# Optimization experiments

Hardware: AMD Instinct MI355X
Metric: run time of the kernel (lower is better)

Reference implementation:

```python
import jax, jax.numpy as jnp
import numpy as np

D_MODEL = 768
N_HEADS = 12
HEAD_DIM = D_MODEL // N_HEADS
D_FF = 4 * D_MODEL
EPS = 1e-5


def setup_inputs() -> dict:
    key = jax.random.key(0)
    ks = jax.random.split(key, 16)
    s = 0.02
    x = jax.random.normal(ks[0], (2, 2048, D_MODEL), dtype=jnp.float32)
    wq = jax.random.normal(ks[1], (D_MODEL, D_MODEL), dtype=jnp.float32) * s
    bq = jnp.zeros((D_MODEL,), jnp.float32)
    wk = jax.random.normal(ks[2], (D_MODEL, D_MODEL), dtype=jnp.float32) * s
    bk = jnp.zeros((D_MODEL,), jnp.float32)
    wv = jax.random.normal(ks[3], (D_MODEL, D_MODEL), dtype=jnp.float32) * s
    bv = jnp.zeros((D_MODEL,), jnp.float32)
    wo = jax.random.normal(ks[4], (D_MODEL, D_MODEL), dtype=jnp.float32) * s
    bo = jnp.zeros((D_MODEL,), jnp.float32)
    w1 = jax.random.normal(ks[5], (D_MODEL, D_FF), dtype=jnp.float32) * s
    b1 = jnp.zeros((D_FF,), jnp.float32)
    w2 = jax.random.normal(ks[6], (D_FF, D_MODEL), dtype=jnp.float32) * s
    b2 = jnp.zeros((D_MODEL,), jnp.float32)
    ln1_g = jnp.ones((D_MODEL,), jnp.float32)
    ln1_b = jnp.zeros((D_MODEL,), jnp.float32)
    ln2_g = jnp.ones((D_MODEL,), jnp.float32)
    ln2_b = jnp.zeros((D_MODEL,), jnp.float32)
    return dict(x=x, wq=wq, bq=bq, wk=wk, bk=bk, wv=wv, bv=bv, wo=wo, bo=bo,
                w1=w1, b1=b1, w2=w2, b2=b2,
                ln1_g=ln1_g, ln1_b=ln1_b, ln2_g=ln2_g, ln2_b=ln2_b)


def _layernorm(x, g, b):
    mu = jnp.mean(x, axis=-1, keepdims=True)
    var = jnp.mean(jnp.square(x - mu), axis=-1, keepdims=True)
    return (x - mu) * jax.lax.rsqrt(var + EPS) * g + b


def _attention(x, wq, bq, wk, bk, wv, bv, wo, bo):
    B, S, D = x.shape
    def split_heads(t):  # [B,S,D] -> [B,H,S,Hd]
        return t.reshape(B, S, N_HEADS, HEAD_DIM).transpose(0, 2, 1, 3)
    q = split_heads(x @ wq + bq)
    k = split_heads(x @ wk + bk)
    v = split_heads(x @ wv + bv)
    scores = jnp.einsum('bhqd,bhkd->bhqk', q, k) / np.sqrt(HEAD_DIM).astype(np.float32)
    causal = jnp.tril(jnp.ones((S, S), dtype=bool))
    scores = jnp.where(causal, scores, -jnp.inf)
    weights = jax.nn.softmax(scores, axis=-1)
    attn = jnp.einsum('bhqk,bhkd->bhqd', weights, v)
    attn = attn.transpose(0, 2, 1, 3).reshape(B, S, D)
    return attn @ wo + bo


def reference(x, wq, bq, wk, bk, wv, bv, wo, bo, w1, b1, w2, b2,
              ln1_g, ln1_b, ln2_g, ln2_b):
    x = x + _attention(_layernorm(x, ln1_g, ln1_b), wq, bq, wk, bk, wv, bv, wo, bo)
    h = _layernorm(x, ln2_g, ln2_b)
    ff = jax.nn.relu(h @ w1 + b1) @ w2 + b2
    return x + ff
```

## Files before the change

### kernel.cpp

```cpp
#include <hip/hip_runtime.h>
#include <stdint.h>

typedef __bf16 bf16;
typedef float f32x4 __attribute__((ext_vector_type(4)));
typedef bf16 bf16x8 __attribute__((ext_vector_type(8)));
typedef bf16 bf16x4 __attribute__((ext_vector_type(4)));

#define MFMA16(a, b, c) __builtin_amdgcn_mfma_f32_16x16x32_bf16((a), (b), (c), 0, 0, 0)

static __device__ __forceinline__ void load_lds16(const bf16* g, bf16* l) {
  __builtin_amdgcn_global_load_lds(
      (const __attribute__((address_space(1))) void*)g,
      (__attribute__((address_space(3))) void*)l, 16, 0, 0);
}

static __device__ __forceinline__ float fast_exp2(float x) {
#if __has_builtin(__builtin_amdgcn_exp2f)
  return __builtin_amdgcn_exp2f(x);
#else
  return exp2f(x);
#endif
}

__global__ void __launch_bounds__(256) k_transpose(
    const float* s0, const float* s1, const float* s2, const float* s3,
    const float* s4, const float* s5,
    bf16* d0, bf16* d1, bf16* d2, bf16* d3, bf16* d4, bf16* d5) {
  int z = blockIdx.z;
  const float* src; bf16* dst; int R, C;
  switch (z) {
    case 0: src = s0; dst = d0; R = 768;  C = 768;  break;
    case 1: src = s1; dst = d1; R = 768;  C = 768;  break;
    case 2: src = s2; dst = d2; R = 768;  C = 768;  break;
    case 3: src = s3; dst = d3; R = 768;  C = 768;  break;
    case 4: src = s4; dst = d4; R = 768;  C = 3072; break;
    default: src = s5; dst = d5; R = 3072; C = 768; break;
  }
  int tcn = C >> 5;
  int nt = (R >> 5) * tcn;
  int t = blockIdx.x;
  if (t >= nt) return;
  int tr = t / tcn, tc = t % tcn;
  __shared__ float tile[32][33];
  int tx = threadIdx.x & 31, ty = threadIdx.x >> 5;
  for (int i = 0; i < 4; i++)
    tile[ty + i * 8][tx] = src[(size_t)(tr * 32 + ty + i * 8) * C + tc * 32 + tx];
  __syncthreads();
  for (int i = 0; i < 4; i++)
    dst[(size_t)(tc * 32 + ty + i * 8) * R + tr * 32 + tx] = (bf16)tile[tx][ty + i * 8];
}

__global__ void __launch_bounds__(256) k_layernorm(
    const float* __restrict__ in, const float* __restrict__ gam,
    const float* __restrict__ bet, bf16* __restrict__ out) {
  int row = blockIdx.x, tid = threadIdx.x;
  const float* rp = in + (size_t)row * 768;
  float v0 = rp[tid], v1 = rp[tid + 256], v2 = rp[tid + 512];
  float s = v0 + v1 + v2, sq = v0 * v0 + v1 * v1 + v2 * v2;
  for (int off = 1; off < 64; off <<= 1) {
    s += __shfl_xor(s, off, 64);
    sq += __shfl_xor(sq, off, 64);
  }
  __shared__ float ps[8];
  if ((tid & 63) == 0) { ps[tid >> 6] = s; ps[4 + (tid >> 6)] = sq; }
  __syncthreads();
  s = ps[0] + ps[1] + ps[2] + ps[3];
  sq = ps[4] + ps[5] + ps[6] + ps[7];
  float mu = s * (1.0f / 768.0f);
  float rstd = rsqrtf(sq * (1.0f / 768.0f) - mu * mu + 1e-5f);
  bf16* op = out + (size_t)row * 768;
  op[tid] = (bf16)((v0 - mu) * rstd * gam[tid] + bet[tid]);
  op[tid + 256] = (bf16)((v1 - mu) * rstd * gam[tid + 256] + bet[tid + 256]);
  op[tid + 512] = (bf16)((v2 - mu) * rstd * gam[tid + 512] + bet[tid + 512]);
}

__global__ void __launch_bounds__(256) k_ln2_reduce(
    const bf16* __restrict__ p0, const bf16* __restrict__ p1,
    const bf16* __restrict__ p2, const bf16* __restrict__ p3,
    const float* __restrict__ x, const float* __restrict__ bo,
    const float* __restrict__ gam, const float* __restrict__ bet,
    float* __restrict__ x1, bf16* __restrict__ h2) {
  int row = blockIdx.x, tid = threadIdx.x;
  size_t base = (size_t)row * 768;
  float v0, v1, v2;
  {
    size_t c = base + tid;
    v0 = (float)p0[c] + (float)p1[c] + (float)p2[c] + (float)p3[c] + x[c] + bo[tid];
    c = base + tid + 256;
    v1 = (float)p0[c] + (float)p1[c] + (float)p2[c] + (float)p3[c] + x[c] + bo[tid + 256];
    c = base + tid + 512;
    v2 = (float)p0[c] + (float)p1[c] + (float)p2[c] + (float)p3[c] + x[c] + bo[tid + 512];
  }
  x1[base + tid] = v0; x1[base + tid + 256] = v1; x1[base + tid + 512] = v2;
  float s = v0 + v1 + v2, sq = v0 * v0 + v1 * v1 + v2 * v2;
  for (int off = 1; off < 64; off <<= 1) {
    s += __shfl_xor(s, off, 64);
    sq += __shfl_xor(sq, off, 64);
  }
  __shared__ float ps[8];
  if ((tid & 63) == 0) { ps[tid >> 6] = s; ps[4 + (tid >> 6)] = sq; }
  __syncthreads();
  s = ps[0] + ps[1] + ps[2] + ps[3];
  sq = ps[4] + ps[5] + ps[6] + ps[7];
  float mu = s * (1.0f / 768.0f);
  float rstd = rsqrtf(sq * (1.0f / 768.0f) - mu * mu + 1e-5f);
  bf16* op = h2 + base;
  op[tid] = (bf16)((v0 - mu) * rstd * gam[tid] + bet[tid]);
  op[tid + 256] = (bf16)((v1 - mu) * rstd * gam[tid + 256] + bet[tid + 256]);
  op[tid + 512] = (bf16)((v2 - mu) * rstd * gam[tid + 512] + bet[tid + 512]);
}

static __device__ __forceinline__ f32x4 cvt4(const bf16* p, size_t i) {
  bf16x4 v = *(const bf16x4*)(p + i);
  f32x4 r;
  for (int j = 0; j < 4; j++) r[j] = (float)v[j];
  return r;
}

__global__ void __launch_bounds__(256) k_ff2_reduce(
    const bf16* __restrict__ f0, const bf16* __restrict__ f1,
    const bf16* __restrict__ f2, const bf16* __restrict__ f3,
    const float* __restrict__ x1, const float* __restrict__ b2,
    float* __restrict__ out) {
  size_t i = ((size_t)blockIdx.x * 256 + threadIdx.x) * 4;
  int col = (int)(i % 768);
  f32x4 v = *(const f32x4*)(x1 + i);
  f32x4 b = *(const f32x4*)(b2 + col);
  f32x4 r = v + b + cvt4(f0, i) + cvt4(f1, i) + cvt4(f2, i) + cvt4(f3, i);
  *(f32x4*)(out + i) = r;
}

static __device__ __forceinline__ void gemm_core(
    const bf16* __restrict__ A, int lda, const bf16* __restrict__ Bt, int ldb,
    int Kc, int m0, int n0, bf16* As, bf16* Bs, f32x4 acc[4][4]) {
  int tid = threadIdx.x, w = tid >> 6, lane = tid & 63, quad = lane >> 4, l15 = lane & 15;
  int wr = w >> 1, wc = w & 1;
  int srow = lane & 15, skc = (lane >> 4) * 8;
  const bf16* ga[2];
  const bf16* gb[2];
  for (int c = 0; c < 2; c++) {
    int seg = w * 2 + c;
    ga[c] = A + (size_t)(m0 + seg * 16 + srow) * lda + skc;
    gb[c] = Bt + (size_t)(n0 + seg * 16 + srow) * ldb + skc;
  }
  bf16x8 rA[2][2], rB[2][2];
  for (int c = 0; c < 2; c++)
    for (int h = 0; h < 2; h++) {
      rA[c][h] = *(const bf16x8*)(ga[c] + h * 32);
      rB[c][h] = *(const bf16x8*)(gb[c] + h * 32);
    }
  int k0 = 0;
  while (true) {
    for (int c = 0; c < 2; c++) {
      int seg = w * 2 + c;
      for (int h = 0; h < 2; h++) {
        *(bf16x8*)(As + seg * 1024 + h * 512 + lane * 8) = rA[c][h];
        *(bf16x8*)(Bs + seg * 1024 + h * 512 + lane * 8) = rB[c][h];
      }
    }
    __syncthreads();
    bool more = (k0 + 64) < Kc;
    if (more) {
      for (int c = 0; c < 2; c++)
        for (int h = 0; h < 2; h++) {
          rA[c][h] = *(const bf16x8*)(ga[c] + k0 + 64 + h * 32);
          rB[c][h] = *(const bf16x8*)(gb[c] + k0 + 64 + h * 32);
        }
    }
    for (int ks = 0; ks < 2; ks++) {
      bf16x8 af[4], bfr[4];
      for (int mi = 0; mi < 4; mi++)
        af[mi] = *(const bf16x8*)(As + (wr * 4 + mi) * 1024 + ks * 512 + quad * 128 + l15 * 8);
      for (int ni = 0; ni < 4; ni++)
        bfr[ni] = *(const bf16x8*)(Bs + (wc * 4 + ni) * 1024 + ks * 512 + quad * 128 + l15 * 8);
      for (int mi = 0; mi < 4; mi++)
        for (int ni = 0; ni < 4; ni++)
          acc[mi][ni] = MFMA16(af[mi], bfr[ni], acc[mi][ni]);
    }
    k0 += 64;
    if (!more) break;
    __syncthreads();
  }
}

__global__ void __launch_bounds__(256) k_gemm_relu(
    const bf16* __restrict__ A, const bf16* __restrict__ Bt,
    const float* __restrict__ bias, bf16* __restrict__ outp, int K_, int N_) {
  __shared__ __align__(16) bf16 As[128 * 64];
  __shared__ __align__(16) bf16 Bs[128 * 64];
  int m0 = blockIdx.y * 128, n0 = blockIdx.x * 128;
  f32x4 acc[4][4] = {};
  gemm_core(A, K_, Bt, K_, K_, m0, n0, As, Bs, acc);
  int tid = threadIdx.x, w = tid >> 6, lane = tid & 63, quad = lane >> 4, l15 = lane & 15;
  int wr = w >> 1, wc = w & 1;
  float bv[4];
  for (int ni = 0; ni < 4; ni++) bv[ni] = bias[n0 + wc * 64 + ni * 16 + l15];
  for (int mi = 0; mi < 4; mi++) {
    int mb = m0 + wr * 64 + mi * 16 + quad * 4;
    for (int ni = 0; ni < 4; ni++) {
      int n = n0 + wc * 64 + ni * 16 + l15;
      for (int r = 0; r < 4; r++)
        outp[(size_t)(mb + r) * N_ + n] = (bf16)fmaxf(acc[mi][ni][r] + bv[ni], 0.0f);
    }
  }
}

__global__ void __launch_bounds__(256) k_gemm_split(
    const bf16* __restrict__ A, const bf16* __restrict__ Bt,
    bf16* __restrict__ f0, bf16* __restrict__ f1,
    bf16* __restrict__ f2, bf16* __restrict__ f3, int K_, int Kc, int N_) {
  __shared__ __align__(16) bf16 As[128 * 64];
  __shared__ __align__(16) bf16 Bs[128 * 64];
  int z = blockIdx.z;
  bf16* outp = (z == 0) ? f0 : (z == 1) ? f1 : (z == 2) ? f2 : f3;
  int m0 = blockIdx.y * 128, n0 = blockIdx.x * 128;
  f32x4 acc[4][4] = {};
  gemm_core(A + (size_t)z * Kc, K_, Bt + (size_t)z * Kc, K_, Kc, m0, n0, As, Bs, acc);
  int tid = threadIdx.x, w = tid >> 6, lane = tid & 63, quad = lane >> 4, l15 = lane & 15;
  int wr = w >> 1, wc = w & 1;
  for (int mi = 0; mi < 4; mi++) {
    int mb = m0 + wr * 64 + mi * 16 + quad * 4;
    for (int ni = 0; ni < 4; ni++) {
      int n = n0 + wc * 64 + ni * 16 + l15;
      for (int r = 0; r < 4; r++)
        outp[(size_t)(mb + r) * N_ + n] = (bf16)acc[mi][ni][r];
    }
  }
}

__global__ void __launch_bounds__(256) k_gemm_qkv(
    const bf16* __restrict__ h1, const bf16* __restrict__ wqT,
    const bf16* __restrict__ wkT, const bf16* __restrict__ wvT,
    const float* __restrict__ bq, const float* __restrict__ bk,
    const float* __restrict__ bv, bf16* __restrict__ qb,
    bf16* __restrict__ kb, bf16* __restrict__ vtb) {
  __shared__ __align__(16) bf16 As[128 * 64];
  __shared__ __align__(16) bf16 Bs[128 * 64];
  int z = blockIdx.z;
  const bf16* Bt = (z == 0) ? wqT : (z == 1) ? wkT : wvT;
  const float* bias = (z == 0) ? bq : (z == 1) ? bk : bv;
  int m0 = blockIdx.y * 128, n0 = blockIdx.x * 128;
  f32x4 acc[4][4] = {};
  gemm_core(h1, 768, Bt, 768, 768, m0, n0, As, Bs, acc);
  int tid = threadIdx.x, w = tid >> 6, lane = tid & 63, quad = lane >> 4, l15 = lane & 15;
  int wr = w >> 1, wc = w & 1;
  float bvv[4];
  for (int ni = 0; ni < 4; ni++) bvv[ni] = bias[n0 + wc * 64 + ni * 16 + l15];
  for (int mi = 0; mi < 4; mi++) {
    int mb = m0 + wr * 64 + mi * 16 + quad * 4;
    int b = mb >> 11, s0_ = mb & 2047;
    for (int ni = 0; ni < 4; ni++) {
      int n = n0 + wc * 64 + ni * 16 + l15;
      int h = n >> 6, hd = n & 63;
      if (z < 2) {
        bf16* outp = (z == 0) ? qb : kb;
        size_t base = (size_t)(b * 12 + h) * 2048 * 64;
        for (int r = 0; r < 4; r++)
          outp[base + (size_t)(s0_ + r) * 64 + hd] = (bf16)(acc[mi][ni][r] + bvv[ni]);
      } else {
        bf16x4 pk;
        for (int r = 0; r < 4; r++) pk[r] = (bf16)(acc[mi][ni][r] + bvv[ni]);
        *(bf16x4*)(vtb + (((size_t)(b * 12 + h) * 64 + hd) * 2048 + s0_)) = pk;
      }
    }
  }
}

__global__ void __launch_bounds__(256) k_attn(
    const bf16* __restrict__ qb, const bf16* __restrict__ kb,
    const bf16* __restrict__ vtb, bf16* __restrict__ out) {
  __shared__ __align__(16) bf16 Ks[128 * 64];
  __shared__ __align__(16) bf16 Vs[64 * 128];
  __shared__ __align__(16) bf16 Ps[4][16 * 128];
  int qt = 31 - (blockIdx.x / 24);
  int bh = blockIdx.x % 24;
  int q0 = qt * 64;
  int tid = threadIdx.x, w = tid >> 6, lane = tid & 63, quad = lane >> 4, l15 = lane & 15;
  const bf16* qbase = qb + (size_t)bh * 2048 * 64;
  const bf16* kbase = kb + (size_t)bh * 2048 * 64;
  const bf16* vbase = vtb + (size_t)bh * 64 * 2048;

  bf16x8 qf[2];
  for (int ds = 0; ds < 2; ds++)
    qf[ds] = *(const bf16x8*)(qbase + (size_t)(q0 + w * 16 + l15) * 64 + ds * 32 + quad * 8);

  f32x4 o[4] = {};
  f32x4 l_i = {};

  const float C2 = 0.18033688011112042f;
  int nkt = (qt >> 1) + 1;
  for (int kt = 0; kt < nkt; kt++) {
    int k0 = kt * 128;
    __syncthreads();
    {
      int rsub = lane >> 3, c8 = lane & 7;
      for (int c = 0; c < 4; c++) {
        int seg = c * 4 + w;
        int row = seg * 8 + rsub;
        load_lds16(kbase + (size_t)(k0 + row) * 64 + ((c8 ^ (row & 7)) * 8), Ks + seg * 512);
      }
      int rsub2 = lane >> 4, c16 = lane & 15;
      for (int c = 0; c < 4; c++) {
        int seg = c * 4 + w;
        int row = seg * 4 + rsub2;
        load_lds16(vbase + (size_t)row * 2048 + k0 + ((c16 ^ (row & 15)) * 8), Vs + seg * 512);
      }
    }
    __syncthreads();

    f32x4 sc[8] = {};
    for (int kj = 0; kj < 8; kj++) {
      int krow = kj * 16 + l15;
      for (int ds = 0; ds < 2; ds++) {
        bf16x8 kf = *(const bf16x8*)(Ks + krow * 64 + (((ds * 4 + quad) ^ (krow & 7)) * 8));
        sc[kj] = MFMA16(qf[ds], kf, sc[kj]);
      }
    }
    if (kt == nkt - 1) {
      int qg = q0 + w * 16 + quad * 4;
      for (int kj = 0; kj < 8; kj++) {
        int kg = k0 + kj * 16 + l15;
        for (int r = 0; r < 4; r++)
          if (kg > qg + r) sc[kj][r] = -3.0e38f;
      }
    }
    for (int kj = 0; kj < 8; kj++)
      for (int r = 0; r < 4; r++) {
        float p = fast_exp2(sc[kj][r] * C2);
        sc[kj][r] = p;
        l_i[r] += p;
      }
    for (int kj = 0; kj < 8; kj++) {
      int colb = kj * 16 + l15;
      int chb = colb >> 3, cin = colb & 7;
      for (int r = 0; r < 4; r++) {
        int prow = quad * 4 + r;
        Ps[w][prow * 128 + ((chb ^ prow) * 8) + cin] = (bf16)sc[kj][r];
      }
    }
    for (int ks = 0; ks < 4; ks++) {
      int prow = l15;
      bf16x8 pf = *(const bf16x8*)(&Ps[w][prow * 128 + (((ks * 4 + quad) ^ prow) * 8)]);
      for (int dj = 0; dj < 4; dj++) {
        int vrow = dj * 16 + l15;
        bf16x8 vf = *(const bf16x8*)(Vs + vrow * 128 + (((ks * 4 + quad) ^ (vrow & 15)) * 8));
        o[dj] = MFMA16(pf, vf, o[dj]);
      }
    }
  }
  for (int off = 1; off < 16; off <<= 1)
    for (int r = 0; r < 4; r++) l_i[r] += __shfl_xor(l_i[r], off, 64);
  int b = bh / 12, h = bh % 12;
  f32x4 rl;
  for (int r = 0; r < 4; r++) rl[r] = 1.0f / l_i[r];
  int srow = q0 + w * 16 + quad * 4;
  for (int dj = 0; dj < 4; dj++) {
    int d = h * 64 + dj * 16 + l15;
    for (int r = 0; r < 4; r++)
      out[(size_t)(b * 2048 + srow + r) * 768 + d] = (bf16)(o[dj][r] * rl[r]);
  }
}

extern "C" void kernel_launch(void* const* d_in, const int* in_sizes, int n_in,
                              void* d_out, int out_size, void* d_ws, size_t ws_size,
                              hipStream_t stream) {
  const float* x    = (const float*)d_in[0];
  const float* wq   = (const float*)d_in[1];
  const float* bq   = (const float*)d_in[2];
  const float* wk   = (const float*)d_in[3];
  const float* bk   = (const float*)d_in[4];
  const float* wv   = (const float*)d_in[5];
  const float* bv   = (const float*)d_in[6];
  const float* wo   = (const float*)d_in[7];
  const float* bo   = (const float*)d_in[8];
  const float* w1   = (const float*)d_in[9];
  const float* b1   = (const float*)d_in[10];
  const float* w2   = (const float*)d_in[11];
  const float* b2   = (const float*)d_in[12];
  const float* ln1g = (const float*)d_in[13];
  const float* ln1b = (const float*)d_in[14];
  const float* ln2g = (const float*)d_in[15];
  const float* ln2b = (const float*)d_in[16];

  char* p = (char*)d_ws;
  bf16* wqT = (bf16*)p; p += (size_t)768 * 768 * 2;
  bf16* wkT = (bf16*)p; p += (size_t)768 * 768 * 2;
  bf16* wvT = (bf16*)p; p += (size_t)768 * 768 * 2;
  bf16* woT = (bf16*)p; p += (size_t)768 * 768 * 2;
  bf16* w1T = (bf16*)p; p += (size_t)768 * 3072 * 2;
  bf16* w2T = (bf16*)p; p += (size_t)768 * 3072 * 2;
  bf16* h1   = (bf16*)p; p += (size_t)4096 * 768 * 2;
  bf16* qbuf = (bf16*)p; p += (size_t)4096 * 768 * 2;
  bf16* kbuf = (bf16*)p; p += (size_t)4096 * 768 * 2;
  bf16* vtb  = (bf16*)p; p += (size_t)4096 * 768 * 2;
  bf16* att  = (bf16*)p; p += (size_t)4096 * 768 * 2;
  float* x1  = (float*)p; p += (size_t)4096 * 768 * 4;
  bf16* h2   = (bf16*)p; p += (size_t)4096 * 768 * 2;
  bf16* ffm  = (bf16*)p; p += (size_t)4096 * 3072 * 2;
  bf16* pex  = (bf16*)p; p += (size_t)4096 * 768 * 2;
  bf16* p0 = h1;
  bf16* p1 = qbuf;
  bf16* p2 = kbuf;
  bf16* p3 = pex;
  bf16* f0 = h1; bf16* f1 = qbuf; bf16* f2 = kbuf; bf16* f3 = vtb;

  k_transpose<<<dim3(2304, 1, 6), dim3(256), 0, stream>>>(
      wq, wk, wv, wo, w1, w2, wqT, wkT, wvT, woT, w1T, w2T);
  k_layernorm<<<dim3(4096), dim3(256), 0, stream>>>(x, ln1g, ln1b, h1);
  k_gemm_qkv<<<dim3(6, 32, 3), dim3(256), 0, stream>>>(
      h1, wqT, wkT, wvT, bq, bk, bv, qbuf, kbuf, vtb);
  k_attn<<<dim3(768), dim3(256), 0, stream>>>(qbuf, kbuf, vtb, att);
  k_gemm_split<<<dim3(6, 32, 4), dim3(256), 0, stream>>>(
      att, woT, p0, p1, p2, p3, 768, 192, 768);
  k_ln2_reduce<<<dim3(4096), dim3(256), 0, stream>>>(
      p0, p1, p2, p3, x, bo, ln2g, ln2b, x1, h2);
  k_gemm_relu<<<dim3(24, 32), dim3(256), 0, stream>>>(
      h2, w1T, b1, ffm, 768, 3072);
  k_gemm_split<<<dim3(6, 32, 4), dim3(256), 0, stream>>>(
      ffm, w2T, f0, f1, f2, f3, 3072, 768, 768);
  k_ff2_reduce<<<dim3(3072), dim3(256), 0, stream>>>(
      f0, f1, f2, f3, x1, b2, (float*)d_out);
}
```

Before: 317.0 us.

## Fuse LN1 into prep, fuse FF2 split-K reduce via atomic counters, remap blocks per XCD

Folds the first layernorm into the weight-transpose launch as an extra grid slice, removing one launch. The FF2 split-K reduction moves into the GEMM itself: the last of the four K-split blocks per tile, detected with an atomic counter, sums the partials with the residual and bias. Launch overhead and the separate reduce pass go away, at the cost of fences and atomics; the counters are reset inside the relu GEMM. All GEMMs switch to a 1D grid with an XCD-aware tile mapping so blocks that share A rows land on the same XCD for L2 reuse.

```diff
diff --git a/kernel.cpp b/kernel.cpp
--- a/kernel.cpp
+++ b/kernel.cpp
@@ -22,11 +22,35 @@
 #endif
 }
 
-__global__ void __launch_bounds__(256) k_transpose(
+__global__ void __launch_bounds__(256) k_prep(
     const float* s0, const float* s1, const float* s2, const float* s3,
     const float* s4, const float* s5,
-    bf16* d0, bf16* d1, bf16* d2, bf16* d3, bf16* d4, bf16* d5) {
+    bf16* d0, bf16* d1, bf16* d2, bf16* d3, bf16* d4, bf16* d5,
+    const float* x, const float* ln1g, const float* ln1b, bf16* h1) {
   int z = blockIdx.z;
+  int tid = threadIdx.x;
+  if (z == 6) {
+    int row = blockIdx.x;
+    const float* rp = x + (size_t)row * 768;
+    float v0 = rp[tid], v1 = rp[tid + 256], v2 = rp[tid + 512];
+    float s = v0 + v1 + v2, sq = v0 * v0 + v1 * v1 + v2 * v2;
+    for (int off = 1; off < 64; off <<= 1) {
+      s += __shfl_xor(s, off, 64);
+      sq += __shfl_xor(sq, off, 64);
+    }
+    __shared__ float ps[8];
+    if ((tid & 63) == 0) { ps[tid >> 6] = s; ps[4 + (tid >> 6)] = sq; }
+    __syncthreads();
+    s = ps[0] + ps[1] + ps[2] + ps[3];
+    sq = ps[4] + ps[5] + ps[6] + ps[7];
+    float mu = s * (1.0f / 768.0f);
+    float rstd = rsqrtf(sq * (1.0f / 768.0f) - mu * mu + 1e-5f);
+    bf16* op = h1 + (size_t)row * 768;
+    op[tid] = (bf16)((v0 - mu) * rstd * ln1g[tid] + ln1b[tid]);
+    op[tid + 256] = (bf16)((v1 - mu) * rstd * ln1g[tid + 256] + ln1b[tid + 256]);
+    op[tid + 512] = (bf16)((v2 - mu) * rstd * ln1g[tid + 512] + ln1b[tid + 512]);
+    return;
+  }
   const float* src; bf16* dst; int R, C;
   switch (z) {
     case 0: src = s0; dst = d0; R = 768;  C = 768;  break;
@@ -42,36 +66,12 @@
   if (t >= nt) return;
   int tr = t / tcn, tc = t % tcn;
   __shared__ float tile[32][33];
-  int tx = threadIdx.x & 31, ty = threadIdx.x >> 5;
+  int tx = tid & 31, ty = tid >> 5;
   for (int i = 0; i < 4; i++)
     tile[ty + i * 8][tx] = src[(size_t)(tr * 32 + ty + i * 8) * C + tc * 32 + tx];
   __syncthreads();
   for (int i = 0; i < 4; i++)
     dst[(size_t)(tc * 32 + ty + i * 8) * R + tr * 32 + tx] = (bf16)tile[tx][ty + i * 8];
-}
-
-__global__ void __launch_bounds__(256) k_layernorm(
-    const float* __restrict__ in, const float* __restrict__ gam,
-    const float* __restrict__ bet, bf16* __restrict__ out) {
-  int row = blockIdx.x, tid = threadIdx.x;
-  const float* rp = in + (size_t)row * 768;
-  float v0 = rp[tid], v1 = rp[tid + 256], v2 = rp[tid + 512];
-  float s = v0 + v1 + v2, sq = v0 * v0 + v1 * v1 + v2 * v2;
-  for (int off = 1; off < 64; off <<= 1) {
-    s += __shfl_xor(s, off, 64);
-    sq += __shfl_xor(sq, off, 64);
-  }
-  __shared__ float ps[8];
-  if ((tid & 63) == 0) { ps[tid >> 6] = s; ps[4 + (tid >> 6)] = sq; }
-  __syncthreads();
-  s = ps[0] + ps[1] + ps[2] + ps[3];
-  sq = ps[4] + ps[5] + ps[6] + ps[7];
-  float mu = s * (1.0f / 768.0f);
-  float rstd = rsqrtf(sq * (1.0f / 768.0f) - mu * mu + 1e-5f);
-  bf16* op = out + (size_t)row * 768;
-  op[tid] = (bf16)((v0 - mu) * rstd * gam[tid] + bet[tid]);
-  op[tid + 256] = (bf16)((v1 - mu) * rstd * gam[tid + 256] + bet[tid + 256]);
-  op[tid + 512] = (bf16)((v2 - mu) * rstd * gam[tid + 512] + bet[tid + 512]);
 }
 
 __global__ void __launch_bounds__(256) k_ln2_reduce(
@@ -110,26 +110,6 @@
   op[tid + 512] = (bf16)((v2 - mu) * rstd * gam[tid + 512] + bet[tid + 512]);
 }
 
-static __device__ __forceinline__ f32x4 cvt4(const bf16* p, size_t i) {
-  bf16x4 v = *(const bf16x4*)(p + i);
-  f32x4 r;
-  for (int j = 0; j < 4; j++) r[j] = (float)v[j];
-  return r;
-}
-
-__global__ void __launch_bounds__(256) k_ff2_reduce(
-    const bf16* __restrict__ f0, const bf16* __restrict__ f1,
-    const bf16* __restrict__ f2, const bf16* __restrict__ f3,
-    const float* __restrict__ x1, const float* __restrict__ b2,
-    float* __restrict__ out) {
-  size_t i = ((size_t)blockIdx.x * 256 + threadIdx.x) * 4;
-  int col = (int)(i % 768);
-  f32x4 v = *(const f32x4*)(x1 + i);
-  f32x4 b = *(const f32x4*)(b2 + col);
-  f32x4 r = v + b + cvt4(f0, i) + cvt4(f1, i) + cvt4(f2, i) + cvt4(f3, i);
-  *(f32x4*)(out + i) = r;
-}
-
 static __device__ __forceinline__ void gemm_core(
     const bf16* __restrict__ A, int lda, const bf16* __restrict__ Bt, int ldb,
     int Kc, int m0, int n0, bf16* As, bf16* Bs, f32x4 acc[4][4]) {
@@ -185,10 +165,14 @@
 
 __global__ void __launch_bounds__(256) k_gemm_relu(
     const bf16* __restrict__ A, const bf16* __restrict__ Bt,
-    const float* __restrict__ bias, bf16* __restrict__ outp, int K_, int N_) {
+    const float* __restrict__ bias, bf16* __restrict__ outp,
+    int* __restrict__ cnt, int K_, int N_) {
+  if (blockIdx.x < 192) cnt[blockIdx.x] = 0;
   __shared__ __align__(16) bf16 As[128 * 64];
   __shared__ __align__(16) bf16 Bs[128 * 64];
-  int m0 = blockIdx.y * 128, n0 = blockIdx.x * 128;
+  int l = blockIdx.x, xcd = l & 7, i = l >> 3;
+  int m0 = ((xcd << 2) | (i & 3)) * 128;
+  int n0 = (i >> 2) * 128;
   f32x4 acc[4][4] = {};
   gemm_core(A, K_, Bt, K_, K_, m0, n0, As, Bs, acc);
   int tid = threadIdx.x, w = tid >> 6, lane = tid & 63, quad = lane >> 4, l15 = lane & 15;
@@ -211,9 +195,12 @@
     bf16* __restrict__ f2, bf16* __restrict__ f3, int K_, int Kc, int N_) {
   __shared__ __align__(16) bf16 As[128 * 64];
   __shared__ __align__(16) bf16 Bs[128 * 64];
-  int z = blockIdx.z;
+  int l = blockIdx.x, xcd = l & 7, i = l >> 3;
+  int m0 = ((xcd << 2) | (i & 3)) * 128;
+  int rest = i >> 2;
+  int n0 = (rest % 6) * 128;
+  int z = rest / 6;
   bf16* outp = (z == 0) ? f0 : (z == 1) ? f1 : (z == 2) ? f2 : f3;
-  int m0 = blockIdx.y * 128, n0 = blockIdx.x * 128;
   f32x4 acc[4][4] = {};
   gemm_core(A + (size_t)z * Kc, K_, Bt + (size_t)z * Kc, K_, Kc, m0, n0, As, Bs, acc);
   int tid = threadIdx.x, w = tid >> 6, lane = tid & 63, quad = lane >> 4, l15 = lane & 15;
@@ -225,6 +212,66 @@
       for (int r = 0; r < 4; r++)
         outp[(size_t)(mb + r) * N_ + n] = (bf16)acc[mi][ni][r];
     }
+  }
+}
+
+__global__ void __launch_bounds__(256) k_gemm_ff2(
+    const bf16* __restrict__ A, const bf16* __restrict__ Bt,
+    bf16* __restrict__ f0, bf16* __restrict__ f1,
+    bf16* __restrict__ f2, bf16* __restrict__ f3,
+    const float* __restrict__ x1, const float* __restrict__ b2,
+    float* __restrict__ out, int* __restrict__ cnt, int K_, int Kc, int N_) {
+  __shared__ __align__(16) bf16 As[128 * 64];
+  __shared__ __align__(16) bf16 Bs[128 * 64];
+  int l = blockIdx.x, xcd = l & 7, i = l >> 3;
+  int m_t = (xcd << 2) | (i & 3);
+  int rest = i >> 2;
+  int n_t = rest % 6;
+  int z = rest / 6;
+  int m0 = m_t * 128, n0 = n_t * 128;
+  bf16* outp = (z == 0) ? f0 : (z == 1) ? f1 : (z == 2) ? f2 : f3;
+  f32x4 acc[4][4] = {};
+  gemm_core(A + (size_t)z * Kc, K_, Bt + (size_t)z * Kc, K_, Kc, m0, n0, As, Bs, acc);
+  int tid = threadIdx.x, w = tid >> 6, lane = tid & 63, quad = lane >> 4, l15 = lane & 15;
+  int wr = w >> 1, wc = w & 1;
+  for (int mi = 0; mi < 4; mi++) {
+    int mb = m0 + wr * 64 + mi * 16 + quad * 4;
+    for (int ni = 0; ni < 4; ni++) {
+      int n = n0 + wc * 64 + ni * 16 + l15;
+      for (int r = 0; r < 4; r++)
+        outp[(size_t)(mb + r) * N_ + n] = (bf16)acc[mi][ni][r];
+    }
+  }
+  __threadfence();
+  __syncthreads();
+  int old = 0;
+  if (tid == 0) {
+    old = __hip_atomic_fetch_add(&cnt[n_t + 6 * m_t], 1, __ATOMIC_ACQ_REL,
+                                 __HIP_MEMORY_SCOPE_AGENT);
+  }
+  __shared__ int lastFlag;
+  if (tid == 0) lastFlag = (old == 3) ? 1 : 0;
+  __syncthreads();
+  if (!lastFlag) return;
+  for (int it = 0; it < 8; it++) {
+    int idx = it * 2048 + tid * 8;
+    int r = idx >> 7, c = idx & 127;
+    size_t off = (size_t)(m0 + r) * N_ + n0 + c;
+    bf16x8 a0 = *(const bf16x8*)(f0 + off);
+    bf16x8 a1 = *(const bf16x8*)(f1 + off);
+    bf16x8 a2 = *(const bf16x8*)(f2 + off);
+    bf16x8 a3 = *(const bf16x8*)(f3 + off);
+    f32x4 v0 = *(const f32x4*)(x1 + off);
+    f32x4 v1 = *(const f32x4*)(x1 + off + 4);
+    f32x4 bb0 = *(const f32x4*)(b2 + n0 + c);
+    f32x4 bb1 = *(const f32x4*)(b2 + n0 + c + 4);
+    f32x4 r0, r1;
+    for (int j = 0; j < 4; j++) {
+      r0[j] = v0[j] + bb0[j] + (float)a0[j] + (float)a1[j] + (float)a2[j] + (float)a3[j];
+      r1[j] = v1[j] + bb1[j] + (float)a0[j + 4] + (float)a1[j + 4] + (float)a2[j + 4] + (float)a3[j + 4];
+    }
+    *(f32x4*)(out + off) = r0;
+    *(f32x4*)(out + off + 4) = r1;
   }
 }
 
@@ -236,10 +283,13 @@
     bf16* __restrict__ kb, bf16* __restrict__ vtb) {
   __shared__ __align__(16) bf16 As[128 * 64];
   __shared__ __align__(16) bf16 Bs[128 * 64];
-  int z = blockIdx.z;
+  int l = blockIdx.x, xcd = l & 7, i = l >> 3;
+  int m0 = ((xcd << 2) | (i & 3)) * 128;
+  int rest = i >> 2;
+  int n0 = (rest % 6) * 128;
+  int z = rest / 6;
   const bf16* Bt = (z == 0) ? wqT : (z == 1) ? wkT : wvT;
   const float* bias = (z == 0) ? bq : (z == 1) ? bk : bv;
-  int m0 = blockIdx.y * 128, n0 = blockIdx.x * 128;
   f32x4 acc[4][4] = {};
   gemm_core(h1, 768, Bt, 768, 768, m0, n0, As, Bs, acc);
   int tid = threadIdx.x, w = tid >> 6, lane = tid & 63, quad = lane >> 4, l15 = lane & 15;
@@ -398,26 +448,25 @@
   bf16* h2   = (bf16*)p; p += (size_t)4096 * 768 * 2;
   bf16* ffm  = (bf16*)p; p += (size_t)4096 * 3072 * 2;
   bf16* pex  = (bf16*)p; p += (size_t)4096 * 768 * 2;
+  int* cnt   = (int*)p;  p += 192 * sizeof(int);
   bf16* p0 = h1;
   bf16* p1 = qbuf;
   bf16* p2 = kbuf;
   bf16* p3 = pex;
   bf16* f0 = h1; bf16* f1 = qbuf; bf16* f2 = kbuf; bf16* f3 = vtb;
 
-  k_transpose<<<dim3(2304, 1, 6), dim3(256), 0, stream>>>(
-      wq, wk, wv, wo, w1, w2, wqT, wkT, wvT, woT, w1T, w2T);
-  k_layernorm<<<dim3(4096), dim3(256), 0, stream>>>(x, ln1g, ln1b, h1);
-  k_gemm_qkv<<<dim3(6, 32, 3), dim3(256), 0, stream>>>(
+  k_prep<<<dim3(4096, 1, 7), dim3(256), 0, stream>>>(
+      wq, wk, wv, wo, w1, w2, wqT, wkT, wvT, woT, w1T, w2T,
+      x, ln1g, ln1b, h1);
+  k_gemm_qkv<<<dim3(576), dim3(256), 0, stream>>>(
       h1, wqT, wkT, wvT, bq, bk, bv, qbuf, kbuf, vtb);
   k_attn<<<dim3(768), dim3(256), 0, stream>>>(qbuf, kbuf, vtb, att);
-  k_gemm_split<<<dim3(6, 32, 4), dim3(256), 0, stream>>>(
+  k_gemm_split<<<dim3(768), dim3(256), 0, stream>>>(
       att, woT, p0, p1, p2, p3, 768, 192, 768);
   k_ln2_reduce<<<dim3(4096), dim3(256), 0, stream>>>(
       p0, p1, p2, p3, x, bo, ln2g, ln2b, x1, h2);
-  k_gemm_relu<<<dim3(24, 32), dim3(256), 0, stream>>>(
-      h2, w1T, b1, ffm, 768, 3072);
-  k_gemm_split<<<dim3(6, 32, 4), dim3(256), 0, stream>>>(
-      ffm, w2T, f0, f1, f2, f3, 3072, 768, 768);
-  k_ff2_reduce<<<dim3(3072), dim3(256), 0, stream>>>(
-      f0, f1, f2, f3, x1, b2, (float*)d_out);
-}
+  k_gemm_relu<<<dim3(768), dim3(256), 0, stream>>>(
+      h2, w1T, b1, ffm, cnt, 768, 3072);
+  k_gemm_ff2<<<dim3(768), dim3(256), 0, stream>>>(
+      ffm, w2T, f0, f1, f2, f3, x1, b2, (float*)d_out, cnt, 3072, 768, 768);
+}
```

Measured after the change: 440.1 us. 1.39x slower.
